# Kernel optimization log

Hardware: AMD Instinct MI355X
Metric: run time of the kernel (lower is better)

## Reference

```python
import jax, jax.numpy as jnp
import numpy as np

N_ATOMS = 1_000_000
NUM_STRUCTURES = 10_000  # static n_structures (torch uses batch.max()+1)
HIDDEN = 128
IN_DIM = 4
NUM_HID_LAYERS = 2  # num_layers - 1 extra hidden linears


def setup_inputs() -> dict:
    key = jax.random.key(0)
    ks = jax.random.split(key, 12)
    positions = jax.random.normal(ks[0], (N_ATOMS, 3), dtype=jnp.float32)
    atomic_numbers = jax.random.randint(ks[1], (N_ATOMS,), 1, 100, dtype=jnp.int32)
    batch = jnp.sort(jax.random.randint(ks[2], (N_ATOMS,), 0, NUM_STRUCTURES, dtype=jnp.int32))
    s = 0.05
    W_in = jax.random.normal(ks[3], (IN_DIM, HIDDEN), dtype=jnp.float32) * s
    b_in = jnp.zeros((HIDDEN,), dtype=jnp.float32)
    W_h = jax.random.normal(ks[4], (NUM_HID_LAYERS, HIDDEN, HIDDEN), dtype=jnp.float32) * s
    b_h = jnp.zeros((NUM_HID_LAYERS, HIDDEN), dtype=jnp.float32)
    W_e = jax.random.normal(ks[5], (HIDDEN, 1), dtype=jnp.float32) * s
    b_e = jnp.zeros((1,), dtype=jnp.float32)
    W_s = jax.random.normal(ks[6], (HIDDEN, 6), dtype=jnp.float32) * s
    b_s = jnp.zeros((6,), dtype=jnp.float32)
    return {"positions": positions, "atomic_numbers": atomic_numbers, "batch": batch,
            "W_in": W_in, "b_in": b_in, "W_h": W_h, "b_h": b_h,
            "W_e": W_e, "b_e": b_e, "W_s": W_s, "b_s": b_s}


def reference(positions, atomic_numbers, batch, W_in, b_in, W_h, b_h, W_e, b_e, W_s, b_s):
    # per-atom features: [pos(3), Z(1)] -> [N, 4]
    feats = jnp.concatenate([positions, atomic_numbers.astype(jnp.float32)[:, None]], axis=-1)
    h = jax.nn.silu(feats @ W_in + b_in)          # [N, H]
    for i in range(W_h.shape[0]):                 # small fixed layer count
        h = jax.nn.silu(h @ W_h[i] + b_h[i])
    atom_energies = (h @ W_e + b_e)[:, 0]         # [N]
    # one fused segment-sum replaces the O(S) python masked-sum loop
    energies = jax.ops.segment_sum(atom_energies, batch, num_segments=NUM_STRUCTURES)
    forces = jnp.zeros_like(positions)            # positions.requires_grad is False in fwd path
    stress = h.mean(axis=0) @ W_s + b_s           # [6]
    return energies, forces, stress
```

## Files before the change

kernel.cpp:

```cpp
#include <hip/hip_runtime.h>

#define HID 128
#define TPB 256
#define NBLOCKS 768

typedef __attribute__((ext_vector_type(8))) short short8v;
typedef __attribute__((ext_vector_type(16))) float f32x16;

__device__ __forceinline__ float bf2f(unsigned short u) {
    return __uint_as_float(((unsigned int)u) << 16);
}
__device__ __forceinline__ unsigned short f2bf(float f) {
    unsigned int u = __float_as_uint(f);
    return (unsigned short)((u + 0x7FFFu + ((u >> 16) & 1u)) >> 16);
}
__device__ __forceinline__ float silu(float x) {
    return x / (1.0f + __expf(-x));
}
__device__ __forceinline__ int swz(int m, int k) {
    return (m * HID + k) ^ ((m & 15) << 3);
}

#define LOADW(dst, off0) { \
    short8v a_; \
    _Pragma("unroll") \
    for (int i = 0; i < 8; ++i) a_[i] = (short)f2bf(W_h[(off0) + i * HID]); \
    dst = a_; }

#define MSTEP(Areg, s, HSRC) { \
    const int k0_ = 16 * (s) + 8 * hi; \
    const short8v Ba_ = *reinterpret_cast<const short8v*>(&HSRC[swz(lm, k0_)]); \
    const short8v Bb_ = *reinterpret_cast<const short8v*>(&HSRC[swz(32 + lm, k0_)]); \
    acc0 = __builtin_amdgcn_mfma_f32_32x32x16_bf16(Areg, Ba_, acc0, 0, 0, 0); \
    acc1 = __builtin_amdgcn_mfma_f32_32x32x16_bf16(Areg, Bb_, acc1, 0, 0, 0); }

__global__ __launch_bounds__(TPB, 2) void mlp_kernel(
    const float* __restrict__ pos, const int* __restrict__ anum,
    const int* __restrict__ batch,
    const float* __restrict__ W_in, const float* __restrict__ b_in,
    const float* __restrict__ W_h, const float* __restrict__ b_h,
    const float* __restrict__ W_e, const float* __restrict__ b_e,
    const float* __restrict__ W_s,
    float* __restrict__ out_energies,
    float* __restrict__ ws6,
    int nAtoms)
{
    __shared__ unsigned short h1[64 * HID];
    __shared__ unsigned short h2[64 * HID];
    __shared__ float featsL[64][4];
    __shared__ float bh0L[HID], bh1L[HID], WeL[HID];
    __shared__ float WsL[HID][8];
    __shared__ float ered[4 * 64];

    const int t    = threadIdx.x;
    const int lane = t & 63;
    const int w    = t >> 6;
    const int hi   = lane >> 5;
    const int lm   = lane & 31;
    const int Fw   = 32 * w;

    if (t < HID) {
        bh0L[t] = b_h[t];
        bh1L[t] = b_h[HID + t];
        WeL[t]  = W_e[t];
        #pragma unroll
        for (int c = 0; c < 6; ++c) WsL[t][c] = W_s[t * 6 + c];
    }

    const int j    = t & 127;
    const int slab = t >> 7;
    const float wi0 = W_in[0 * HID + j], wi1 = W_in[1 * HID + j];
    const float wi2 = W_in[2 * HID + j], wi3 = W_in[3 * HID + j];
    const float bin = b_in[j];
    const float be  = b_e[0];

    short8v A00, A01, A02, A03, A04, A05, A06, A07;
    short8v A10, A11, A12, A13, A14, A15, A16, A17;
    {
        const int fc = Fw + lm;
        const int o0 = 8 * hi * HID + fc;
        const int o1 = HID * HID + o0;
        LOADW(A00, o0 +  0 * 16 * HID);  LOADW(A01, o0 +  1 * 16 * HID);
        LOADW(A02, o0 +  2 * 16 * HID);  LOADW(A03, o0 +  3 * 16 * HID);
        LOADW(A04, o0 +  4 * 16 * HID);  LOADW(A05, o0 +  5 * 16 * HID);
        LOADW(A06, o0 +  6 * 16 * HID);  LOADW(A07, o0 +  7 * 16 * HID);
        LOADW(A10, o1 +  0 * 16 * HID);  LOADW(A11, o1 +  1 * 16 * HID);
        LOADW(A12, o1 +  2 * 16 * HID);  LOADW(A13, o1 +  3 * 16 * HID);
        LOADW(A14, o1 +  4 * 16 * HID);  LOADW(A15, o1 +  5 * 16 * HID);
        LOADW(A16, o1 +  6 * 16 * HID);  LOADW(A17, o1 +  7 * 16 * HID);
    }

    float sacc[6] = {0.f, 0.f, 0.f, 0.f, 0.f, 0.f};

    const int nTiles = (nAtoms + 63) >> 6;
    for (int tile = blockIdx.x; tile < nTiles; tile += gridDim.x) {
        const int base = tile << 6;
        __syncthreads();

        if (t < 192) {
            int idx = base * 3 + t;
            const int gmax = nAtoms * 3 - 1;
            if (idx > gmax) idx = gmax;
            featsL[t / 3][t % 3] = pos[idx];
        } else if (t < 256) {
            const int a = t - 192;
            int ga = base + a; if (ga >= nAtoms) ga = nAtoms - 1;
            featsL[a][3] = (float)anum[ga];
        }
        __syncthreads();

        #pragma unroll 4
        for (int ai = 0; ai < 32; ++ai) {
            const int a = 32 * slab + ai;
            const float4 ft = *reinterpret_cast<const float4*>(&featsL[a][0]);
            const float z = fmaf(wi0, ft.x, fmaf(wi1, ft.y,
                            fmaf(wi2, ft.z, fmaf(wi3, ft.w, bin))));
            h1[swz(a, j)] = f2bf(silu(z));
        }
        __syncthreads();

        f32x16 acc0, acc1;
        #pragma unroll
        for (int r = 0; r < 16; ++r) {
            const float b = bh0L[Fw + (r & 3) + 8 * (r >> 2) + 4 * hi];
            acc0[r] = b; acc1[r] = b;
        }
        MSTEP(A00, 0, h1)  MSTEP(A01, 1, h1)  MSTEP(A02, 2, h1)  MSTEP(A03, 3, h1)
        MSTEP(A04, 4, h1)  MSTEP(A05, 5, h1)  MSTEP(A06, 6, h1)  MSTEP(A07, 7, h1)

        #pragma unroll
        for (int g = 0; g < 4; ++g) {
            const int f0 = Fw + 8 * g + 4 * hi;
            ushort4 pa, pb;
            pa.x = f2bf(silu(acc0[4*g+0])); pa.y = f2bf(silu(acc0[4*g+1]));
            pa.z = f2bf(silu(acc0[4*g+2])); pa.w = f2bf(silu(acc0[4*g+3]));
            pb.x = f2bf(silu(acc1[4*g+0])); pb.y = f2bf(silu(acc1[4*g+1]));
            pb.z = f2bf(silu(acc1[4*g+2])); pb.w = f2bf(silu(acc1[4*g+3]));
            *reinterpret_cast<ushort4*>(&h2[swz(lm,      f0)]) = pa;
            *reinterpret_cast<ushort4*>(&h2[swz(32 + lm, f0)]) = pb;
        }
        __syncthreads();

        #pragma unroll
        for (int r = 0; r < 16; ++r) {
            const float b = bh1L[Fw + (r & 3) + 8 * (r >> 2) + 4 * hi];
            acc0[r] = b; acc1[r] = b;
        }
        MSTEP(A10, 0, h2)  MSTEP(A11, 1, h2)  MSTEP(A12, 2, h2)  MSTEP(A13, 3, h2)
        MSTEP(A14, 4, h2)  MSTEP(A15, 5, h2)  MSTEP(A16, 6, h2)  MSTEP(A17, 7, h2)

        const bool v0 = (base + lm)      < nAtoms;
        const bool v1 = (base + 32 + lm) < nAtoms;
        float e0 = 0.f, e1 = 0.f;
        #pragma unroll
        for (int r = 0; r < 16; ++r) {
            const int f = Fw + (r & 3) + 8 * (r >> 2) + 4 * hi;
            const float h3a = silu(acc0[r]);
            const float h3b = silu(acc1[r]);
            const float we = WeL[f];
            e0 = fmaf(h3a, we, e0);
            e1 = fmaf(h3b, we, e1);
            const float hs = (v0 ? h3a : 0.f) + (v1 ? h3b : 0.f);
            #pragma unroll
            for (int c = 0; c < 6; ++c) sacc[c] = fmaf(hs, WsL[f][c], sacc[c]);
        }
        e0 += __shfl_xor(e0, 32);
        e1 += __shfl_xor(e1, 32);
        const float ev = (lane < 32) ? e0 : e1;
        ered[w * 64 + lane] = ev;
        __syncthreads();

        if (w == 0) {
            float e = ered[lane] + ered[64 + lane] + ered[128 + lane] + ered[192 + lane] + be;
            const int ga = base + lane;
            int key = (ga < nAtoms) ? batch[ga] : -1;
            if (key < 0) e = 0.f;
            #pragma unroll
            for (int d = 1; d < 64; d <<= 1) {
                const float eo = __shfl_down(e, d);
                const int   ko = __shfl_down(key, d);
                const bool valid = ((lane + d) < 64) && (ko == key);
                e += valid ? eo : 0.f;
            }
            const int kprev = __shfl_up(key, 1);
            const bool head = (lane == 0) || (kprev != key);
            if (head && key >= 0) atomicAdd(&out_energies[key], e);
        }
    }

    #pragma unroll
    for (int c = 0; c < 6; ++c) {
        float v = sacc[c];
        #pragma unroll
        for (int d = 1; d < 64; d <<= 1) v += __shfl_xor(v, d);
        if (lane == 0) atomicAdd(&ws6[c], v);
    }
}

__global__ void stress_kernel(const float* __restrict__ ws6,
                              const float* __restrict__ b_s,
                              float* __restrict__ out_stress, float invN)
{
    const int c = threadIdx.x;
    if (c < 6) out_stress[c] = fmaf(ws6[c], invN, b_s[c]);
}

extern "C" void kernel_launch(void* const* d_in, const int* in_sizes, int n_in,
                              void* d_out, int out_size, void* d_ws, size_t ws_size,
                              hipStream_t stream) {
    const float* pos  = (const float*)d_in[0];
    const int*   anum = (const int*)d_in[1];
    const int*   batch= (const int*)d_in[2];
    const float* W_in = (const float*)d_in[3];
    const float* b_in = (const float*)d_in[4];
    const float* W_h  = (const float*)d_in[5];
    const float* b_h  = (const float*)d_in[6];
    const float* W_e  = (const float*)d_in[7];
    const float* b_e  = (const float*)d_in[8];
    const float* W_s  = (const float*)d_in[9];
    const float* b_s  = (const float*)d_in[10];

    float* out = (float*)d_out;
    const int nAtoms  = in_sizes[2];
    const int nStruct = out_size - 3 * nAtoms - 6;
    float* ws6 = (float*)d_ws;

    hipMemsetAsync(d_out, 0, (size_t)out_size * sizeof(float), stream);
    hipMemsetAsync(d_ws, 0, 32, stream);

    mlp_kernel<<<NBLOCKS, TPB, 0, stream>>>(pos, anum, batch, W_in, b_in, W_h, b_h,
                                            W_e, b_e, W_s, out, ws6, nAtoms);
    stress_kernel<<<1, 64, 0, stream>>>(ws6, b_s,
                                        out + (size_t)nStruct + 3 * (size_t)nAtoms,
                                        1.0f / (float)nAtoms);
}
```

Measured before the change: 511.0 us.

## Compute input layer with MFMA and defer stress projection to end

The scalar first layer (4->128) is replaced by one MFMA per 32-atom half, with features loaded straight from global memory into registers. This removes the featsL shared staging and one barrier per tile. The per-tile 6-column stress FMA is replaced by a per-register running sum of h3 that is projected through W_s once after the loop. This cuts VALU work per tile. The cost is extra registers for hsum, and bf16 rounding of positions and atomic numbers (up to 99) in the input layer, which adds precision error.

Measured after the change: 442.4 us. -13.4%, faster.

```diff
diff --git a/kernel.cpp b/kernel.cpp
--- a/kernel.cpp
+++ b/kernel.cpp
@@ -7,9 +7,6 @@
 typedef __attribute__((ext_vector_type(8))) short short8v;
 typedef __attribute__((ext_vector_type(16))) float f32x16;
 
-__device__ __forceinline__ float bf2f(unsigned short u) {
-    return __uint_as_float(((unsigned int)u) << 16);
-}
 __device__ __forceinline__ unsigned short f2bf(float f) {
     unsigned int u = __float_as_uint(f);
     return (unsigned short)((u + 0x7FFFu + ((u >> 16) & 1u)) >> 16);
@@ -33,6 +30,19 @@
     const short8v Bb_ = *reinterpret_cast<const short8v*>(&HSRC[swz(32 + lm, k0_)]); \
     acc0 = __builtin_amdgcn_mfma_f32_32x32x16_bf16(Areg, Ba_, acc0, 0, 0, 0); \
     acc1 = __builtin_amdgcn_mfma_f32_32x32x16_bf16(Areg, Bb_, acc1, 0, 0, 0); }
+
+#define PACK_STORE(DST, ACCA, ACCB) \
+    _Pragma("unroll") \
+    for (int g = 0; g < 4; ++g) { \
+        const int f0 = Fw + 8 * g + 4 * hi; \
+        ushort4 pa, pb; \
+        pa.x = f2bf(silu(ACCA[4*g+0])); pa.y = f2bf(silu(ACCA[4*g+1])); \
+        pa.z = f2bf(silu(ACCA[4*g+2])); pa.w = f2bf(silu(ACCA[4*g+3])); \
+        pb.x = f2bf(silu(ACCB[4*g+0])); pb.y = f2bf(silu(ACCB[4*g+1])); \
+        pb.z = f2bf(silu(ACCB[4*g+2])); pb.w = f2bf(silu(ACCB[4*g+3])); \
+        *reinterpret_cast<ushort4*>(&DST[swz(lm,      f0)]) = pa; \
+        *reinterpret_cast<ushort4*>(&DST[swz(32 + lm, f0)]) = pb; \
+    }
 
 __global__ __launch_bounds__(TPB, 2) void mlp_kernel(
     const float* __restrict__ pos, const int* __restrict__ anum,
@@ -47,8 +57,7 @@
 {
     __shared__ unsigned short h1[64 * HID];
     __shared__ unsigned short h2[64 * HID];
-    __shared__ float featsL[64][4];
-    __shared__ float bh0L[HID], bh1L[HID], WeL[HID];
+    __shared__ float binL[HID], bh0L[HID], bh1L[HID], WeL[HID];
     __shared__ float WsL[HID][8];
     __shared__ float ered[4 * 64];
 
@@ -60,22 +69,18 @@
     const int Fw   = 32 * w;
 
     if (t < HID) {
+        binL[t] = b_in[t];
         bh0L[t] = b_h[t];
         bh1L[t] = b_h[HID + t];
         WeL[t]  = W_e[t];
         #pragma unroll
         for (int c = 0; c < 6; ++c) WsL[t][c] = W_s[t * 6 + c];
     }
-
-    const int j    = t & 127;
-    const int slab = t >> 7;
-    const float wi0 = W_in[0 * HID + j], wi1 = W_in[1 * HID + j];
-    const float wi2 = W_in[2 * HID + j], wi3 = W_in[3 * HID + j];
-    const float bin = b_in[j];
-    const float be  = b_e[0];
+    const float be = b_e[0];
 
     short8v A00, A01, A02, A03, A04, A05, A06, A07;
     short8v A10, A11, A12, A13, A14, A15, A16, A17;
+    short8v Ain;
     {
         const int fc = Fw + lm;
         const int o0 = 8 * hi * HID + fc;
@@ -88,38 +93,50 @@
         LOADW(A12, o1 +  2 * 16 * HID);  LOADW(A13, o1 +  3 * 16 * HID);
         LOADW(A14, o1 +  4 * 16 * HID);  LOADW(A15, o1 +  5 * 16 * HID);
         LOADW(A16, o1 +  6 * 16 * HID);  LOADW(A17, o1 +  7 * 16 * HID);
-    }
-
-    float sacc[6] = {0.f, 0.f, 0.f, 0.f, 0.f, 0.f};
+        #pragma unroll
+        for (int i = 0; i < 8; ++i) Ain[i] = 0;
+        if (hi == 0) {
+            Ain[0] = (short)f2bf(W_in[0 * HID + fc]);
+            Ain[1] = (short)f2bf(W_in[1 * HID + fc]);
+            Ain[2] = (short)f2bf(W_in[2 * HID + fc]);
+            Ain[3] = (short)f2bf(W_in[3 * HID + fc]);
+        }
+    }
+
+    f32x16 hsum;
+    #pragma unroll
+    for (int r = 0; r < 16; ++r) hsum[r] = 0.f;
 
     const int nTiles = (nAtoms + 63) >> 6;
     for (int tile = blockIdx.x; tile < nTiles; tile += gridDim.x) {
         const int base = tile << 6;
+
+        short8v Fa, Fb;
+        #pragma unroll
+        for (int i = 0; i < 8; ++i) { Fa[i] = 0; Fb[i] = 0; }
+        if (hi == 0) {
+            int ga = base + lm;      if (ga >= nAtoms) ga = nAtoms - 1;
+            int gb = base + 32 + lm; if (gb >= nAtoms) gb = nAtoms - 1;
+            Fa[0] = (short)f2bf(pos[ga * 3 + 0]);
+            Fa[1] = (short)f2bf(pos[ga * 3 + 1]);
+            Fa[2] = (short)f2bf(pos[ga * 3 + 2]);
+            Fa[3] = (short)f2bf((float)anum[ga]);
+            Fb[0] = (short)f2bf(pos[gb * 3 + 0]);
+            Fb[1] = (short)f2bf(pos[gb * 3 + 1]);
+            Fb[2] = (short)f2bf(pos[gb * 3 + 2]);
+            Fb[3] = (short)f2bf((float)anum[gb]);
+        }
+        f32x16 acc0, acc1;
+        #pragma unroll
+        for (int r = 0; r < 16; ++r) {
+            const float b = binL[Fw + (r & 3) + 8 * (r >> 2) + 4 * hi];
+            acc0[r] = b; acc1[r] = b;
+        }
+        acc0 = __builtin_amdgcn_mfma_f32_32x32x16_bf16(Ain, Fa, acc0, 0, 0, 0);
+        acc1 = __builtin_amdgcn_mfma_f32_32x32x16_bf16(Ain, Fb, acc1, 0, 0, 0);
+        PACK_STORE(h1, acc0, acc1)
         __syncthreads();
 
-        if (t < 192) {
-            int idx = base * 3 + t;
-            const int gmax = nAtoms * 3 - 1;
-            if (idx > gmax) idx = gmax;
-            featsL[t / 3][t % 3] = pos[idx];
-        } else if (t < 256) {
-            const int a = t - 192;
-            int ga = base + a; if (ga >= nAtoms) ga = nAtoms - 1;
-            featsL[a][3] = (float)anum[ga];
-        }
-        __syncthreads();
-
-        #pragma unroll 4
-        for (int ai = 0; ai < 32; ++ai) {
-            const int a = 32 * slab + ai;
-            const float4 ft = *reinterpret_cast<const float4*>(&featsL[a][0]);
-            const float z = fmaf(wi0, ft.x, fmaf(wi1, ft.y,
-                            fmaf(wi2, ft.z, fmaf(wi3, ft.w, bin))));
-            h1[swz(a, j)] = f2bf(silu(z));
-        }
-        __syncthreads();
-
-        f32x16 acc0, acc1;
         #pragma unroll
         for (int r = 0; r < 16; ++r) {
             const float b = bh0L[Fw + (r & 3) + 8 * (r >> 2) + 4 * hi];
@@ -127,18 +144,7 @@
         }
         MSTEP(A00, 0, h1)  MSTEP(A01, 1, h1)  MSTEP(A02, 2, h1)  MSTEP(A03, 3, h1)
         MSTEP(A04, 4, h1)  MSTEP(A05, 5, h1)  MSTEP(A06, 6, h1)  MSTEP(A07, 7, h1)
-
-        #pragma unroll
-        for (int g = 0; g < 4; ++g) {
-            const int f0 = Fw + 8 * g + 4 * hi;
-            ushort4 pa, pb;
-            pa.x = f2bf(silu(acc0[4*g+0])); pa.y = f2bf(silu(acc0[4*g+1]));
-            pa.z = f2bf(silu(acc0[4*g+2])); pa.w = f2bf(silu(acc0[4*g+3]));
-            pb.x = f2bf(silu(acc1[4*g+0])); pb.y = f2bf(silu(acc1[4*g+1]));
-            pb.z = f2bf(silu(acc1[4*g+2])); pb.w = f2bf(silu(acc1[4*g+3]));
-            *reinterpret_cast<ushort4*>(&h2[swz(lm,      f0)]) = pa;
-            *reinterpret_cast<ushort4*>(&h2[swz(32 + lm, f0)]) = pb;
-        }
+        PACK_STORE(h2, acc0, acc1)
         __syncthreads();
 
         #pragma unroll
@@ -160,9 +166,7 @@
             const float we = WeL[f];
             e0 = fmaf(h3a, we, e0);
             e1 = fmaf(h3b, we, e1);
-            const float hs = (v0 ? h3a : 0.f) + (v1 ? h3b : 0.f);
-            #pragma unroll
-            for (int c = 0; c < 6; ++c) sacc[c] = fmaf(hs, WsL[f][c], sacc[c]);
+            hsum[r] += (v0 ? h3a : 0.f) + (v1 ? h3b : 0.f);
         }
         e0 += __shfl_xor(e0, 32);
         e1 += __shfl_xor(e1, 32);
@@ -188,12 +192,23 @@
         }
     }
 
+    float s0 = 0.f, s1 = 0.f, s2 = 0.f, s3 = 0.f, s4 = 0.f, s5 = 0.f;
     #pragma unroll
-    for (int c = 0; c < 6; ++c) {
-        float v = sacc[c];
-        #pragma unroll
-        for (int d = 1; d < 64; d <<= 1) v += __shfl_xor(v, d);
-        if (lane == 0) atomicAdd(&ws6[c], v);
+    for (int r = 0; r < 16; ++r) {
+        const int f = Fw + (r & 3) + 8 * (r >> 2) + 4 * hi;
+        const float h = hsum[r];
+        s0 = fmaf(h, WsL[f][0], s0); s1 = fmaf(h, WsL[f][1], s1);
+        s2 = fmaf(h, WsL[f][2], s2); s3 = fmaf(h, WsL[f][3], s3);
+        s4 = fmaf(h, WsL[f][4], s4); s5 = fmaf(h, WsL[f][5], s5);
+    }
+    #pragma unroll
+    for (int d = 1; d < 64; d <<= 1) {
+        s0 += __shfl_xor(s0, d); s1 += __shfl_xor(s1, d); s2 += __shfl_xor(s2, d);
+        s3 += __shfl_xor(s3, d); s4 += __shfl_xor(s4, d); s5 += __shfl_xor(s5, d);
+    }
+    if (lane == 0) {
+        atomicAdd(&ws6[0], s0); atomicAdd(&ws6[1], s1); atomicAdd(&ws6[2], s2);
+        atomicAdd(&ws6[3], s3); atomicAdd(&ws6[4], s4); atomicAdd(&ws6[5], s5);
     }
 }
 
```
